# Kernel tuning notes

Measured on AMD Instinct MI355X. Metric: run time of the kernel, lower is better.

Reference implementation:

```python
import jax, jax.numpy as jnp
import numpy as np

G = 7          # gauss_order
Q = G * G      # quadrature points
B1, B2 = 2048, 256
LOG2PI = float(np.log(2.0 * np.pi))


def _quadrature(g):
    # interval (-1,1) x (-1,1): halfwidth=1, mean=0
    eta, w = np.polynomial.legendre.leggauss(g)
    pts = np.stack(np.meshgrid(eta, eta, indexing='ij'), axis=0).reshape(2, -1)  # [2, G^2]
    wts = (w * w[:, None]).ravel()  # [G^2]
    return pts.astype(np.float32), wts.astype(np.float32)


def setup_inputs() -> dict:
    key = jax.random.key(0)
    k1, k2, k3, k4 = jax.random.split(key, 4)
    pts, wts = _quadrature(G)
    tv_means = jax.random.normal(k1, (B1, B2, 2), dtype=jnp.float32)
    # SPD covariances: A @ A^T + eps*I
    A = 0.5 * jax.random.normal(k2, (B1, B2, 2, 2), dtype=jnp.float32)
    tv_covars = A @ jnp.swapaxes(A, -1, -2) + 0.1 * jnp.eye(2, dtype=jnp.float32)
    # proper rotation matrices from random angles
    theta = jax.random.uniform(k3, (B1, B2), dtype=jnp.float32, minval=0.0, maxval=2.0 * np.pi)
    c, s = jnp.cos(theta), jnp.sin(theta)
    rotations = jnp.stack([jnp.stack([c, -s], -1), jnp.stack([s, c], -1)], -2)  # [B1,B2,2,2]
    translations = jax.random.normal(k4, (B1, B2, 2), dtype=jnp.float32)
    return {
        'tv_means': tv_means,
        'tv_covars': tv_covars,
        'rotations': rotations,
        'translations': translations,
        'eta_01': jnp.asarray(pts),
        'weights': jnp.asarray(wts),
    }


def reference(tv_means, tv_covars, rotations, translations, eta_01, weights):
    # gauss_pts: rotate quadrature points, then translate -> [B1,B2,Q,2]
    gauss_pts = jnp.einsum('...ij,jq->...qi', rotations, eta_01) + translations[..., None, :]
    # MVN(tv_means, tv_covars) log_prob, broadcast over quadrature dim.
    diff = gauss_pts - tv_means[..., None, :]               # [B1,B2,Q,2]
    dx, dy = diff[..., 0], diff[..., 1]                      # [B1,B2,Q]
    c00 = tv_covars[..., 0, 0][..., None]
    c01 = tv_covars[..., 0, 1][..., None]
    c10 = tv_covars[..., 1, 0][..., None]
    c11 = tv_covars[..., 1, 1][..., None]
    det = c00 * c11 - c01 * c10                              # [B1,B2,1]
    # Mahalanobis term via closed-form 2x2 inverse
    quad = (c11 * dx * dx - (c01 + c10) * dx * dy + c00 * dy * dy) / det
    logp = -0.5 * quad - LOG2PI - 0.5 * jnp.log(det)         # [B1,B2,Q]
    integral = jnp.clip(jnp.sum(jnp.exp(logp) * weights, axis=-1), 0.0, 1.0)  # [B1,B2]
    return gauss_pts, integral
```

## Files before the change

kernel.cpp:

```cpp
#include <hip/hip_runtime.h>
#include <math.h>

#define LOG2PI_F 1.8378770664093453f

typedef float vf4 __attribute__((ext_vector_type(4)));

__global__ __launch_bounds__(256) void gauss2d_kernel(
    const float* __restrict__ tv_means,
    const float* __restrict__ tv_covars,
    const float* __restrict__ rotations,
    const float* __restrict__ translations,
    const float* __restrict__ eta,
    const float* __restrict__ weights,
    float* __restrict__ gauss_pts,
    float* __restrict__ integral,
    unsigned int B,
    unsigned int partB_blocks)
{
    if (blockIdx.x < partB_blocks) {
        unsigned int p = blockIdx.x * 256u + threadIdx.x;
        if (p >= B) return;

        const float4 R  = ((const float4*)rotations)[p];
        const float2 tr = ((const float2*)translations)[p];
        const float2 mu = ((const float2*)tv_means)[p];
        const float4 C  = ((const float4*)tv_covars)[p];

        float det     = C.x * C.w - C.y * C.z;
        float inv_det = 1.0f / det;
        float lognorm = fmaf(-0.5f, __logf(det), -LOG2PI_F);
        float c01p10  = C.y + C.z;

        float s = 0.0f;
        #pragma unroll 7
        for (int q = 0; q < 49; ++q) {
            float ex = eta[q];
            float ey = eta[49 + q];
            float gx = fmaf(R.x, ex, fmaf(R.y, ey, tr.x));
            float gy = fmaf(R.z, ex, fmaf(R.w, ey, tr.y));
            float dx = gx - mu.x;
            float dy = gy - mu.y;
            float quad = (C.w * dx * dx - c01p10 * dx * dy + C.x * dy * dy) * inv_det;
            s += weights[q] * __expf(fmaf(-0.5f, quad, lognorm));
        }
        integral[p] = fminf(fmaxf(s, 0.0f), 1.0f);
    } else {
        const unsigned int NP = B * 49u;
        unsigned int tid = (blockIdx.x - partB_blocks) * 256u + threadIdx.x;
        unsigned int t0  = tid * 4u;
        if (t0 >= NP) return;

        unsigned int p0 = t0 / 49u;
        unsigned int q0 = t0 - p0 * 49u;

        float4 R0 = ((const float4*)rotations)[p0];
        float2 T0 = ((const float2*)translations)[p0];
        float4 R1 = R0;
        float2 T1 = T0;
        if (q0 >= 46u && p0 + 1u < B) {
            R1 = ((const float4*)rotations)[p0 + 1u];
            T1 = ((const float2*)translations)[p0 + 1u];
        }

        if (t0 + 4u <= NP) {
            float o[8];
            #pragma unroll
            for (int j = 0; j < 4; ++j) {
                unsigned int q = q0 + (unsigned)j;
                bool cross = q >= 49u;
                q = cross ? q - 49u : q;
                float4 R = cross ? R1 : R0;
                float2 T = cross ? T1 : T0;
                float ex = eta[q];
                float ey = eta[49u + q];
                o[2*j]   = fmaf(R.x, ex, fmaf(R.y, ey, T.x));
                o[2*j+1] = fmaf(R.z, ex, fmaf(R.w, ey, T.y));
            }
            vf4* dst = (vf4*)(gauss_pts + (size_t)t0 * 2u);
            vf4 v0 = { o[0], o[1], o[2], o[3] };
            vf4 v1 = { o[4], o[5], o[6], o[7] };
            __builtin_nontemporal_store(v0, dst);
            __builtin_nontemporal_store(v1, dst + 1);
        } else {
            for (unsigned int t = t0; t < NP; ++t) {
                unsigned int q = t - t0 + q0;
                bool cross = q >= 49u;
                q = cross ? q - 49u : q;
                float4 R = cross ? R1 : R0;
                float2 T = cross ? T1 : T0;
                float ex = eta[q];
                float ey = eta[49u + q];
                gauss_pts[(size_t)t*2u]      = fmaf(R.x, ex, fmaf(R.y, ey, T.x));
                gauss_pts[(size_t)t*2u + 1u] = fmaf(R.z, ex, fmaf(R.w, ey, T.y));
            }
        }
    }
}

extern "C" void kernel_launch(void* const* d_in, const int* in_sizes, int n_in,
                              void* d_out, int out_size, void* d_ws, size_t ws_size,
                              hipStream_t stream) {
    const float* tv_means     = (const float*)d_in[0];
    const float* tv_covars    = (const float*)d_in[1];
    const float* rotations    = (const float*)d_in[2];
    const float* translations = (const float*)d_in[3];
    const float* eta          = (const float*)d_in[4];
    const float* weights      = (const float*)d_in[5];

    const unsigned int B = (unsigned int)(in_sizes[0] / 2);
    float* gauss_pts = (float*)d_out;
    float* integral  = (float*)d_out + (size_t)B * 98u;

    const unsigned int partB_blocks = (B + 255u) / 256u;
    const size_t NP = (size_t)B * 49u;
    const unsigned int partA_threads_div4 = (unsigned int)((NP + 3u) / 4u);
    const unsigned int partA_blocks = (partA_threads_div4 + 255u) / 256u;

    dim3 grid(partA_blocks + partB_blocks);
    dim3 block(256);
    hipLaunchKernelGGL(gauss2d_kernel, grid, block, 0, stream,
                       tv_means, tv_covars, rotations, translations,
                       eta, weights, gauss_pts, integral, B, partB_blocks);
}
```

Before: 263.5 us.

## Split fused kernel into separate gauss-points and integral kernels

```diff
diff --git a/kernel.cpp b/kernel.cpp
--- a/kernel.cpp
+++ b/kernel.cpp
@@ -5,96 +5,100 @@
 
 typedef float vf4 __attribute__((ext_vector_type(4)));
 
-__global__ __launch_bounds__(256) void gauss2d_kernel(
+__global__ __launch_bounds__(256) void gauss_pts_kernel(
+    const float* __restrict__ rotations,
+    const float* __restrict__ translations,
+    const float* __restrict__ eta,
+    float* __restrict__ gauss_pts,
+    unsigned int B)
+{
+    const unsigned int NP = B * 49u;
+    unsigned int tid = blockIdx.x * 256u + threadIdx.x;
+    unsigned int t0  = tid * 4u;
+    if (t0 >= NP) return;
+
+    unsigned int p0 = t0 / 49u;
+    unsigned int q0 = t0 - p0 * 49u;
+
+    float4 R0 = ((const float4*)rotations)[p0];
+    float2 T0 = ((const float2*)translations)[p0];
+    float4 R1 = R0;
+    float2 T1 = T0;
+    if (q0 >= 46u && p0 + 1u < B) {
+        R1 = ((const float4*)rotations)[p0 + 1u];
+        T1 = ((const float2*)translations)[p0 + 1u];
+    }
+
+    if (t0 + 4u <= NP) {
+        float o[8];
+        #pragma unroll
+        for (int j = 0; j < 4; ++j) {
+            unsigned int q = q0 + (unsigned)j;
+            bool cross = q >= 49u;
+            q = cross ? q - 49u : q;
+            float4 R = cross ? R1 : R0;
+            float2 T = cross ? T1 : T0;
+            float ex = eta[q];
+            float ey = eta[49u + q];
+            o[2*j]   = fmaf(R.x, ex, fmaf(R.y, ey, T.x));
+            o[2*j+1] = fmaf(R.z, ex, fmaf(R.w, ey, T.y));
+        }
+        vf4* dst = (vf4*)(gauss_pts + (size_t)t0 * 2u);
+        vf4 v0 = { o[0], o[1], o[2], o[3] };
+        vf4 v1 = { o[4], o[5], o[6], o[7] };
+        dst[0] = v0;
+        dst[1] = v1;
+    } else {
+        for (unsigned int t = t0; t < NP; ++t) {
+            unsigned int q = t - t0 + q0;
+            bool cross = q >= 49u;
+            q = cross ? q - 49u : q;
+            float4 R = cross ? R1 : R0;
+            float2 T = cross ? T1 : T0;
+            float ex = eta[q];
+            float ey = eta[49u + q];
+            gauss_pts[(size_t)t*2u]      = fmaf(R.x, ex, fmaf(R.y, ey, T.x));
+            gauss_pts[(size_t)t*2u + 1u] = fmaf(R.z, ex, fmaf(R.w, ey, T.y));
+        }
+    }
+}
+
+__global__ __launch_bounds__(256) void integral_kernel(
     const float* __restrict__ tv_means,
     const float* __restrict__ tv_covars,
     const float* __restrict__ rotations,
     const float* __restrict__ translations,
     const float* __restrict__ eta,
     const float* __restrict__ weights,
-    float* __restrict__ gauss_pts,
     float* __restrict__ integral,
-    unsigned int B,
-    unsigned int partB_blocks)
+    unsigned int B)
 {
-    if (blockIdx.x < partB_blocks) {
-        unsigned int p = blockIdx.x * 256u + threadIdx.x;
-        if (p >= B) return;
+    unsigned int p = blockIdx.x * 256u + threadIdx.x;
+    if (p >= B) return;
 
-        const float4 R  = ((const float4*)rotations)[p];
-        const float2 tr = ((const float2*)translations)[p];
-        const float2 mu = ((const float2*)tv_means)[p];
-        const float4 C  = ((const float4*)tv_covars)[p];
+    const float4 R  = ((const float4*)rotations)[p];
+    const float2 tr = ((const float2*)translations)[p];
+    const float2 mu = ((const float2*)tv_means)[p];
+    const float4 C  = ((const float4*)tv_covars)[p];
 
-        float det     = C.x * C.w - C.y * C.z;
-        float inv_det = 1.0f / det;
-        float lognorm = fmaf(-0.5f, __logf(det), -LOG2PI_F);
-        float c01p10  = C.y + C.z;
+    float det     = C.x * C.w - C.y * C.z;
+    float inv_det = 1.0f / det;
+    float lognorm = fmaf(-0.5f, __logf(det), -LOG2PI_F);
+    float c01p10  = C.y + C.z;
 
-        float s = 0.0f;
-        #pragma unroll 7
-        for (int q = 0; q < 49; ++q) {
-            float ex = eta[q];
-            float ey = eta[49 + q];
-            float gx = fmaf(R.x, ex, fmaf(R.y, ey, tr.x));
-            float gy = fmaf(R.z, ex, fmaf(R.w, ey, tr.y));
-            float dx = gx - mu.x;
-            float dy = gy - mu.y;
-            float quad = (C.w * dx * dx - c01p10 * dx * dy + C.x * dy * dy) * inv_det;
-            s += weights[q] * __expf(fmaf(-0.5f, quad, lognorm));
-        }
-        integral[p] = fminf(fmaxf(s, 0.0f), 1.0f);
-    } else {
-        const unsigned int NP = B * 49u;
-        unsigned int tid = (blockIdx.x - partB_blocks) * 256u + threadIdx.x;
-        unsigned int t0  = tid * 4u;
-        if (t0 >= NP) return;
-
-        unsigned int p0 = t0 / 49u;
-        unsigned int q0 = t0 - p0 * 49u;
-
-        float4 R0 = ((const float4*)rotations)[p0];
-        float2 T0 = ((const float2*)translations)[p0];
-        float4 R1 = R0;
-        float2 T1 = T0;
-        if (q0 >= 46u && p0 + 1u < B) {
-            R1 = ((const float4*)rotations)[p0 + 1u];
-            T1 = ((const float2*)translations)[p0 + 1u];
-        }
-
-        if (t0 + 4u <= NP) {
-            float o[8];
-            #pragma unroll
-            for (int j = 0; j < 4; ++j) {
-                unsigned int q = q0 + (unsigned)j;
-                bool cross = q >= 49u;
-                q = cross ? q - 49u : q;
-                float4 R = cross ? R1 : R0;
-                float2 T = cross ? T1 : T0;
-                float ex = eta[q];
-                float ey = eta[49u + q];
-                o[2*j]   = fmaf(R.x, ex, fmaf(R.y, ey, T.x));
-                o[2*j+1] = fmaf(R.z, ex, fmaf(R.w, ey, T.y));
-            }
-            vf4* dst = (vf4*)(gauss_pts + (size_t)t0 * 2u);
-            vf4 v0 = { o[0], o[1], o[2], o[3] };
-            vf4 v1 = { o[4], o[5], o[6], o[7] };
-            __builtin_nontemporal_store(v0, dst);
-            __builtin_nontemporal_store(v1, dst + 1);
-        } else {
-            for (unsigned int t = t0; t < NP; ++t) {
-                unsigned int q = t - t0 + q0;
-                bool cross = q >= 49u;
-                q = cross ? q - 49u : q;
-                float4 R = cross ? R1 : R0;
-                float2 T = cross ? T1 : T0;
-                float ex = eta[q];
-                float ey = eta[49u + q];
-                gauss_pts[(size_t)t*2u]      = fmaf(R.x, ex, fmaf(R.y, ey, T.x));
-                gauss_pts[(size_t)t*2u + 1u] = fmaf(R.z, ex, fmaf(R.w, ey, T.y));
-            }
-        }
+    float s = 0.0f;
+    #pragma unroll 7
+    for (int q = 0; q < 49; ++q) {
+        float ex = eta[q];
+        float ey = eta[49 + q];
+        float gx = fmaf(R.x, ex, fmaf(R.y, ey, tr.x));
+        float gy = fmaf(R.z, ex, fmaf(R.w, ey, tr.y));
+        float dx = gx - mu.x;
+        float dy = gy - mu.y;
+        float quad = (C.w * dx * dx - c01p10 * dx * dy + C.x * dy * dy) * inv_det;
+        s += weights[q] * __expf(fmaf(-0.5f, quad, lognorm));
     }
+    integral[p] = fminf(fmaxf(s, 0.0f), 1.0f);
 }
 
 extern "C" void kernel_launch(void* const* d_in, const int* in_sizes, int n_in,
@@ -111,14 +115,14 @@
     float* gauss_pts = (float*)d_out;
     float* integral  = (float*)d_out + (size_t)B * 98u;
 
-    const unsigned int partB_blocks = (B + 255u) / 256u;
     const size_t NP = (size_t)B * 49u;
-    const unsigned int partA_threads_div4 = (unsigned int)((NP + 3u) / 4u);
-    const unsigned int partA_blocks = (partA_threads_div4 + 255u) / 256u;
+    const unsigned int ptsThreads = (unsigned int)((NP + 3u) / 4u);
+    const unsigned int ptsBlocks  = (ptsThreads + 255u) / 256u;
+    const unsigned int intBlocks  = (B + 255u) / 256u;
 
-    dim3 grid(partA_blocks + partB_blocks);
-    dim3 block(256);
-    hipLaunchKernelGGL(gauss2d_kernel, grid, block, 0, stream,
+    hipLaunchKernelGGL(gauss_pts_kernel, dim3(ptsBlocks), dim3(256), 0, stream,
+                       rotations, translations, eta, gauss_pts, B);
+    hipLaunchKernelGGL(integral_kernel, dim3(intBlocks), dim3(256), 0, stream,
                        tv_means, tv_covars, rotations, translations,
-                       eta, weights, gauss_pts, integral, B, partB_blocks);
+                       eta, weights, integral, B);
 }
```

Result: slower. 287.2 us (+9.0%).
